# Kernel optimization log

Hardware: AMD Instinct MI355X
Metric: run time of the kernel (lower is better)

The kernel has to match this reference:

```python
import jax, jax.numpy as jnp
import numpy as np

B, L, D, H, DK, DV = 2, 2048, 1024, 16, 64, 64
NEG_INF = -100000000.0


def setup_inputs() -> dict:
    key = jax.random.key(0)
    ks = jax.random.split(key, 10)
    s = 0.02
    inp = {
        "q": jax.random.normal(ks[0], (B, L, D), jnp.float32),
        "k": jax.random.normal(ks[1], (B, L, D), jnp.float32),
        "v": jax.random.normal(ks[2], (B, L, D), jnp.float32),
        "Wq": jax.random.normal(ks[3], (D, H * DK), jnp.float32) * s,
        "bq": jnp.zeros((H * DK,), jnp.float32),
        "Wk": jax.random.normal(ks[4], (D, H * DK), jnp.float32) * s,
        "bk": jnp.zeros((H * DK,), jnp.float32),
        "Wv": jax.random.normal(ks[5], (D, H * DV), jnp.float32) * s,
        "bv": jnp.zeros((H * DV,), jnp.float32),
        "W0": jax.random.normal(ks[6], (H * DV, D), jnp.float32) * s,
        "b0": jnp.zeros((D,), jnp.float32),
        "key_padding_mask": jax.random.uniform(ks[7], (B, L)) < 0.1,
        # 3D causal mask (B, Lq, Lk); True = masked
        "attn_mask": jnp.broadcast_to(jnp.triu(jnp.ones((L, L), bool), k=1), (B, L, L)),
    }
    return inp


def reference(q, k, v, Wq, bq, Wk, bk, Wv, bv, W0, b0, key_padding_mask, attn_mask):
    b, lq, _ = q.shape
    lk = k.shape[1]
    dk = Wq.shape[1] // H
    dv = Wv.shape[1] // H
    qh = (q @ Wq + bq).reshape(b, lq, H, dk)  # (B,Lq,H,dk)
    kh = (k @ Wk + bk).reshape(b, lk, H, dk)
    vh = (v @ Wv + bv).reshape(b, lk, H, dv)
    # scaled scores (B,H,Lq,Lk)
    attn = jnp.einsum("bqhd,bkhd->bhqk", qh, kh) / jnp.sqrt(jnp.float32(dk))
    # attn_mask (B,Lq,Lk): masked_fill semantics
    attn = jnp.where(attn_mask[:, None, :, :], NEG_INF, attn)
    # key_padding_mask (B,Lq): masks full query rows (broadcast over keys)
    attn = jnp.where(key_padding_mask[:, None, :, None], NEG_INF, attn)
    attn = jax.nn.softmax(attn, axis=-1)
    out = jnp.einsum("bhqk,bkhd->bqhd", attn, vh).reshape(b, lq, H * dv)
    out = out @ W0 + b0  # (B,Lq,D)
    return out, attn
```

## Files before the change

### kernel.cpp

```cpp
#include <hip/hip_runtime.h>

#define B_ 2
#define L_ 2048
#define D_ 1024
#define H_ 16
#define DKV 64
#define NEG_INF -1e8f

typedef float f32x4 __attribute__((ext_vector_type(4)));
typedef __bf16 bf16x8 __attribute__((ext_vector_type(8)));
typedef unsigned int u32x4 __attribute__((ext_vector_type(4)));
typedef unsigned int u32x2 __attribute__((ext_vector_type(2)));
typedef unsigned short u16x4 __attribute__((ext_vector_type(4)));

__device__ __forceinline__ unsigned short f2bfbits(float f) {
  unsigned int u = __builtin_bit_cast(unsigned int, f);
  unsigned int r = (u + 0x7FFFu + ((u >> 16) & 1u)) >> 16;
  return (unsigned short)r;
}
__device__ __forceinline__ float bf2f(unsigned short b) {
  unsigned int u = ((unsigned int)b) << 16;
  return __builtin_bit_cast(float, u);
}

__device__ __forceinline__ void gload16(const unsigned short* g, unsigned short* l) {
  __builtin_amdgcn_global_load_lds(
      (const __attribute__((address_space(1))) unsigned int*)g,
      (__attribute__((address_space(3))) unsigned int*)l, 16, 0, 0);
}

template<int N>
__device__ __forceinline__ void waitbar() {
  asm volatile("s_waitcnt vmcnt(%0) lgkmcnt(0)" :: "i"(N) : "memory");
  __builtin_amdgcn_sched_barrier(0);
  __builtin_amdgcn_s_barrier();
}
__device__ __forceinline__ void bar_lgkm() {
  asm volatile("s_waitcnt lgkmcnt(0)" ::: "memory");
  __builtin_amdgcn_sched_barrier(0);
  __builtin_amdgcn_s_barrier();
}

__global__ __launch_bounds__(256) void prep_k(
    const float* __restrict__ xq, const float* __restrict__ xk, const float* __restrict__ xv,
    const float* __restrict__ Wq, const float* __restrict__ Wk,
    const float* __restrict__ Wv, const float* __restrict__ W0,
    const void* __restrict__ kpm_raw,
    unsigned short* __restrict__ oq, unsigned short* __restrict__ ok, unsigned short* __restrict__ ov,
    unsigned short* __restrict__ Wtq, unsigned short* __restrict__ Wtk,
    unsigned short* __restrict__ Wtv, unsigned short* __restrict__ W0t,
    unsigned char* __restrict__ kpmn)
{
  __shared__ float Tl[64][65];
  const int bid = blockIdx.x, tid = threadIdx.x;
  if (bid < 6144) {
    const int proj = bid >> 11;
    const float* X = proj == 0 ? xq : (proj == 1 ? xk : xv);
    unsigned short* O = proj == 0 ? oq : (proj == 1 ? ok : ov);
    const long i8 = ((long)(bid & 2047) * 256 + tid) * 8;
    f32x4 a = *(const f32x4*)(X + i8);
    f32x4 b = *(const f32x4*)(X + i8 + 4);
    u32x4 p;
    p[0] = (unsigned)f2bfbits(a[0]) | ((unsigned)f2bfbits(a[1]) << 16);
    p[1] = (unsigned)f2bfbits(a[2]) | ((unsigned)f2bfbits(a[3]) << 16);
    p[2] = (unsigned)f2bfbits(b[0]) | ((unsigned)f2bfbits(b[1]) << 16);
    p[3] = (unsigned)f2bfbits(b[2]) | ((unsigned)f2bfbits(b[3]) << 16);
    *(u32x4*)(O + i8) = p;
  } else if (bid < 7168) {
    const int wid = bid - 6144;
    const int m = wid >> 8, t = wid & 255;
    const float* W = m == 0 ? Wq : (m == 1 ? Wk : (m == 2 ? Wv : W0));
    unsigned short* Wt = m == 0 ? Wtq : (m == 1 ? Wtk : (m == 2 ? Wtv : W0t));
    const int k0 = ((t >> 4) & 15) * 64, n0 = (t & 15) * 64;
    #pragma unroll
    for (int it = 0; it < 4; ++it) {
      int idx = it * 256 + tid;
      int r = idx >> 4, c4 = (idx & 15) << 2;
      f32x4 x = *(const f32x4*)(W + (long)(k0 + r) * 1024 + n0 + c4);
      Tl[r][c4] = x[0]; Tl[r][c4 + 1] = x[1]; Tl[r][c4 + 2] = x[2]; Tl[r][c4 + 3] = x[3];
    }
    __syncthreads();
    #pragma unroll
    for (int it = 0; it < 2; ++it) {
      int idx = it * 256 + tid;
      int n = idx >> 3, c8 = (idx & 7) << 3;
      u32x4 p;
      #pragma unroll
      for (int j = 0; j < 4; ++j)
        p[j] = (unsigned)f2bfbits(Tl[c8 + 2 * j][n]) | ((unsigned)f2bfbits(Tl[c8 + 2 * j + 1][n]) << 16);
      *(u32x4*)(Wt + (long)(n0 + n) * 1024 + k0 + c8) = p;
    }
  } else {
    __shared__ int flag;
    if (tid == 0) flag = 0;
    __syncthreads();
    const unsigned* w = (const unsigned*)kpm_raw;
    unsigned bad = 0;
    for (int i = tid; i < 1024; i += 256) bad |= (w[i] > 1u) ? 1u : 0u;
    if (bad) flag = 1;
    __syncthreads();
    const bool u8 = (flag != 0);
    const unsigned char* u = (const unsigned char*)kpm_raw;
    for (int i = tid; i < B_ * L_; i += 256)
      kpmn[i] = u8 ? (u[i] != 0) : (w[i] != 0);
  }
}

__global__ __launch_bounds__(256) void qkv_gemm_k(
    const unsigned short* __restrict__ xqb, const unsigned short* __restrict__ xkb,
    const unsigned short* __restrict__ xvb,
    const unsigned short* __restrict__ Wtq, const unsigned short* __restrict__ Wtk,
    const unsigned short* __restrict__ Wtv,
    const float* __restrict__ bq, const float* __restrict__ bk, const float* __restrict__ bv,
    unsigned short* __restrict__ oq, unsigned short* __restrict__ ok, unsigned short* __restrict__ ov,
    float* __restrict__ part)
{
  __shared__ __align__(16) unsigned short Al[128][64];
  __shared__ __align__(16) unsigned short Bl[128][64];
  const int proj = blockIdx.y;
  const unsigned short* X  = proj == 0 ? xqb : (proj == 1 ? xkb : xvb);
  const unsigned short* Wt = proj == 0 ? Wtq : (proj == 1 ? Wtk : Wtv);
  const float* bias = proj == 0 ? bq : (proj == 1 ? bk : bv);
  unsigned short* O = proj == 0 ? oq : (proj == 1 ? ok : ov);
  const int mt = blockIdx.x, zp = blockIdx.z;
  const int bb = zp >> 3, hp = zp & 7;
  const int tid = threadIdx.x, lane = tid & 63, w = tid >> 6, g = lane >> 4, l16 = lane & 15;
  const int wm = w >> 1, wn = w & 1;
  const long arow0 = (long)bb * L_ + mt * 128;
  const long brow0 = (long)hp * 128;
  const int lr8 = lane >> 3, lc = lane & 7;

  const f32x4 zero4 = {0.f, 0.f, 0.f, 0.f};
  f32x4 acc[4][4];
  #pragma unroll
  for (int i = 0; i < 4; ++i)
    #pragma unroll
    for (int j = 0; j < 4; ++j) acc[i][j] = zero4;

  for (int kt = 0; kt < D_; kt += 64) {
    #pragma unroll
    for (int i = 0; i < 4; ++i) {
      int r = w * 32 + i * 8 + lr8;
      gload16(X + (arow0 + r) * D_ + kt + ((lc ^ (r & 7)) << 3), &Al[w * 32 + i * 8][0]);
      gload16(Wt + (brow0 + r) * D_ + kt + ((lc ^ (r & 7)) << 3), &Bl[w * 32 + i * 8][0]);
    }
    __syncthreads();
    #pragma unroll
    for (int ks = 0; ks < 2; ++ks) {
      bf16x8 a[4], bv8[4];
      #pragma unroll
      for (int fm = 0; fm < 4; ++fm) {
        int ra = wm * 64 + fm * 16 + l16;
        a[fm] = *(const bf16x8*)&Al[ra][((ks * 4 + g) ^ (ra & 7)) << 3];
      }
      #pragma unroll
      for (int fn = 0; fn < 4; ++fn) {
        int rb = wn * 64 + fn * 16 + l16;
        bv8[fn] = *(const bf16x8*)&Bl[rb][((ks * 4 + g) ^ (rb & 7)) << 3];
      }
      #pragma unroll
      for (int fm = 0; fm < 4; ++fm)
        #pragma unroll
        for (int fn = 0; fn < 4; ++fn)
          acc[fm][fn] = __builtin_amdgcn_mfma_f32_16x16x32_bf16(a[fm], bv8[fn], acc[fm][fn], 0, 0, 0);
    }
    __syncthreads();
  }
  #pragma unroll
  for (int fm = 0; fm < 4; ++fm)
    #pragma unroll
    for (int fn = 0; fn < 4; ++fn)
      #pragma unroll
      for (int r = 0; r < 4; ++r) {
        int row = mt * 128 + wm * 64 + fm * 16 + g * 4 + r;
        int col = wn * 64 + fn * 16 + l16;
        float val = acc[fm][fn][r] + bias[hp * 128 + col];
        int zh = bb * H_ + hp * 2 + (col >> 6);
        O[(long)zh * L_ * 64 + (long)row * 64 + (col & 63)] = f2bfbits(val);
      }

  if (proj == 2) {
    float* red = (float*)&Al[0][0];
    __syncthreads();
    #pragma unroll
    for (int fn = 0; fn < 4; ++fn) {
      float s = 0.f;
      #pragma unroll
      for (int fm = 0; fm < 4; ++fm)
        #pragma unroll
        for (int r = 0; r < 4; ++r) s += acc[fm][fn][r];
      red[(wm * 4 + g) * 128 + wn * 64 + fn * 16 + l16] = s;
    }
    __syncthreads();
    if (tid < 128) {
      float s = 0.f;
      #pragma unroll
      for (int i = 0; i < 8; ++i) s += red[i * 128 + tid];
      s += 128.f * bias[hp * 128 + tid];
      int zh = bb * H_ + hp * 2 + (tid >> 6);
      part[((long)zh * 16 + mt) * 64 + (tid & 63)] = s;
    }
  }
}

__global__ __launch_bounds__(256) void oproj_gemm_k(
    const unsigned short* __restrict__ Ab, const unsigned short* __restrict__ W0t,
    const float* __restrict__ b0, float* __restrict__ out)
{
  __shared__ __align__(16) unsigned short Al[64][64];
  __shared__ __align__(16) unsigned short Bl[64][64];
  const int mt = blockIdx.x, nt = blockIdx.y;
  const int tid = threadIdx.x, lane = tid & 63, w = tid >> 6, g = lane >> 4, l16 = lane & 15;
  const int wm = w >> 1, wn = w & 1;
  const int lr8 = lane >> 3, lc = lane & 7;

  const f32x4 zero4 = {0.f, 0.f, 0.f, 0.f};
  f32x4 acc[2][2];
  #pragma unroll
  for (int i = 0; i < 2; ++i)
    #pragma unroll
    for (int j = 0; j < 2; ++j) acc[i][j] = zero4;

  for (int kt = 0; kt < D_; kt += 64) {
    #pragma unroll
    for (int i = 0; i < 2; ++i) {
      int r = w * 16 + i * 8 + lr8;
      gload16(Ab + (long)(mt * 64 + r) * D_ + kt + ((lc ^ (r & 7)) << 3), &Al[w * 16 + i * 8][0]);
      gload16(W0t + (long)(nt * 64 + r) * D_ + kt + ((lc ^ (r & 7)) << 3), &Bl[w * 16 + i * 8][0]);
    }
    __syncthreads();
    #pragma unroll
    for (int ks = 0; ks < 2; ++ks) {
      bf16x8 a[2], bv8[2];
      #pragma unroll
      for (int fm = 0; fm < 2; ++fm) {
        int ra = wm * 32 + fm * 16 + l16;
        a[fm] = *(const bf16x8*)&Al[ra][((ks * 4 + g) ^ (ra & 7)) << 3];
      }
      #pragma unroll
      for (int fn = 0; fn < 2; ++fn) {
        int rb = wn * 32 + fn * 16 + l16;
        bv8[fn] = *(const bf16x8*)&Bl[rb][((ks * 4 + g) ^ (rb & 7)) << 3];
      }
      #pragma unroll
      for (int fm = 0; fm < 2; ++fm)
        #pragma unroll
        for (int fn = 0; fn < 2; ++fn)
          acc[fm][fn] = __builtin_amdgcn_mfma_f32_16x16x32_bf16(a[fm], bv8[fn], acc[fm][fn], 0, 0, 0);
    }
    __syncthreads();
  }
  #pragma unroll
  for (int fm = 0; fm < 2; ++fm)
    #pragma unroll
    for (int fn = 0; fn < 2; ++fn)
      #pragma unroll
      for (int r = 0; r < 4; ++r) {
        int row = mt * 64 + wm * 32 + fm * 16 + g * 4 + r;
        int col = nt * 64 + wn * 32 + fn * 16 + l16;
        out[(long)row * D_ + col] = acc[fm][fn][r] + b0[col];
      }
}

__global__ __launch_bounds__(256, 4) void attn_pv_k(
    const unsigned short* __restrict__ qh, const unsigned short* __restrict__ kh,
    const unsigned short* __restrict__ vh, const unsigned char* __restrict__ kpm,
    const float* __restrict__ part, float* __restrict__ attn,
    unsigned short* __restrict__ oh)
{
  __shared__ __align__(16) char smem[64 * 68 * 4];
  auto Ql = (unsigned short (*)[72])smem;
  auto Pl = (float (*)[68])smem;
  __shared__ __align__(16) unsigned short Kl[64][64];
  __shared__ __align__(16) unsigned short Vl[64][72];
  __shared__ unsigned char padl[64];
  __shared__ float csVl[64];

  const int tid = threadIdx.x, lane = tid & 63, w = tid >> 6, g = lane >> 4, l16 = lane & 15;
  const int bid = blockIdx.x;
  const int z = bid & 31;
  const int qq5 = bid >> 5;
  const int sx = (qq5 & 8) ? ((qq5 & 16) ? 55 - qq5 : 23 - qq5) : qq5;
  const int q0 = sx * 64;
  const int b = z >> 4, h = z & 15;
  const long zoff = (long)z * L_ * DKV;
  const int rowbase = q0 + w * 16 + g * 4;

  const int lr8 = lane >> 3, lc = lane & 7;
  const int kr = tid >> 3, kc8 = (tid & 7) << 3;
  const int vk = tid >> 4, vn4 = (tid & 15) << 2;

  #pragma unroll
  for (int it = 0; it < 2; ++it) {
    int f = it * 256 + tid;
    int r = f >> 3, c8 = (f & 7) << 3;
    *(u32x4*)&Ql[r][c8] = *(const u32x4*)(qh + zoff + (long)(q0 + r) * 64 + c8);
  }
  if (tid < 64) {
    padl[tid] = kpm[b * L_ + q0 + tid];
    float s = 0.f;
    #pragma unroll
    for (int m = 0; m < 16; ++m) s += part[((long)z * 16 + m) * 64 + tid];
    csVl[tid] = s;
  }
  __syncthreads();
  bf16x8 a[2];
  #pragma unroll
  for (int ks = 0; ks < 2; ++ks)
    a[ks] = *(const bf16x8*)&Ql[w * 16 + l16][ks * 32 + g * 8];
  bool pad[4];
  #pragma unroll
  for (int r = 0; r < 4; ++r) pad[r] = padl[w * 16 + g * 4 + r] != 0;
  __syncthreads();

  const float invL = 1.0f / (float)L_;

  float psum[4] = {0.f, 0.f, 0.f, 0.f};
  const f32x4 zero4 = {0.f, 0.f, 0.f, 0.f};
  f32x4 o[4];
  #pragma unroll
  for (int fn = 0; fn < 4; ++fn) o[fn] = zero4;

  u16x4 Vreg[4];
  #pragma unroll
  for (int it = 0; it < 4; ++it)
    Vreg[it] = *(const u16x4*)(vh + zoff + (long)(vk + it * 16) * 64 + vn4);
  #pragma unroll
  for (int it = 0; it < 4; ++it) {
    int kk = vk + it * 16;
    int sw = kk ^ (((vn4 >> 2) & 7) << 3);
    Vl[vn4 + 0][sw] = Vreg[it][0]; Vl[vn4 + 1][sw] = Vreg[it][1];
    Vl[vn4 + 2][sw] = Vreg[it][2]; Vl[vn4 + 3][sw] = Vreg[it][3];
  }
  #pragma unroll
  for (int i = 0; i < 2; ++i) {
    int r = w * 16 + i * 8 + lr8;
    gload16(kh + zoff + (long)r * 64 + ((lc ^ (r & 7)) << 3), &Kl[w * 16 + i * 8][0]);
  }
  __builtin_amdgcn_sched_barrier(0);
  if (sx >= 1)
    #pragma unroll
    for (int it = 0; it < 4; ++it)
      Vreg[it] = *(const u16x4*)(vh + zoff + (long)(64 + vk + it * 16) * 64 + vn4);

  for (int kt = 0; kt <= sx; ++kt) {
    if (kt == 0) waitbar<0>(); else waitbar<4>();
    f32x4 s[4];
    #pragma unroll
    for (int fn = 0; fn < 4; ++fn) {
      int fk = fn * 16 + l16;
      bf16x8 bv0 = *(const bf16x8*)&Kl[fk][(g ^ (fk & 7)) << 3];
      bf16x8 bv1 = *(const bf16x8*)&Kl[fk][((4 + g) ^ (fk & 7)) << 3];
      f32x4 t = zero4;
      t = __builtin_amdgcn_mfma_f32_16x16x32_bf16(a[0], bv0, t, 0, 0, 0);
      t = __builtin_amdgcn_mfma_f32_16x16x32_bf16(a[1], bv1, t, 0, 0, 0);
      s[fn] = t;
    }
    #pragma unroll
    for (int fn = 0; fn < 4; ++fn)
      #pragma unroll
      for (int r = 0; r < 4; ++r) {
        int kk = kt * 64 + fn * 16 + l16;
        float sv = s[fn][r] * 0.125f;
        if (kk > rowbase + r) sv = NEG_INF;
        float p = __expf(sv - 12.0f);
        psum[r] += p;
        Pl[w * 16 + g * 4 + r][fn * 16 + l16] = p;
      }
    bf16x8 pa[2];
    #pragma unroll
    for (int ks = 0; ks < 2; ++ks) {
      f32x4 lo = *(const f32x4*)&Pl[w * 16 + l16][ks * 32 + g * 8];
      f32x4 hi = *(const f32x4*)&Pl[w * 16 + l16][ks * 32 + g * 8 + 4];
      bf16x8 t;
      #pragma unroll
      for (int i = 0; i < 4; ++i) { t[i] = (__bf16)lo[i]; t[i + 4] = (__bf16)hi[i]; }
      pa[ks] = t;
    }
    #pragma unroll
    for (int fn = 0; fn < 4; ++fn) {
      int dv = fn * 16 + l16;
      int swz = ((dv >> 2) & 7) << 3;
      bf16x8 vb0 = *(const bf16x8*)&Vl[dv][(0 * 32 + g * 8) ^ swz];
      bf16x8 vb1 = *(const bf16x8*)&Vl[dv][(1 * 32 + g * 8) ^ swz];
      o[fn] = __builtin_amdgcn_mfma_f32_16x16x32_bf16(pa[0], vb0, o[fn], 0, 0, 0);
      o[fn] = __builtin_amdgcn_mfma_f32_16x16x32_bf16(pa[1], vb1, o[fn], 0, 0, 0);
    }
    bar_lgkm();
    if (kt < sx) {
      const unsigned short* kb2 = kh + zoff + (long)((kt + 1) * 64) * 64;
      #pragma unroll
      for (int i = 0; i < 2; ++i) {
        int r = w * 16 + i * 8 + lr8;
        gload16(kb2 + (long)r * 64 + ((lc ^ (r & 7)) << 3), &Kl[w * 16 + i * 8][0]);
      }
      __builtin_amdgcn_sched_barrier(0);
      #pragma unroll
      for (int it = 0; it < 4; ++it) {
        int kk = vk + it * 16;
        int sw = kk ^ (((vn4 >> 2) & 7) << 3);
        Vl[vn4 + 0][sw] = Vreg[it][0]; Vl[vn4 + 1][sw] = Vreg[it][1];
        Vl[vn4 + 2][sw] = Vreg[it][2]; Vl[vn4 + 3][sw] = Vreg[it][3];
      }
      if (kt + 2 <= sx) {
        const long noff = zoff + (long)((kt + 2) * 64) * 64;
        #pragma unroll
        for (int it = 0; it < 4; ++it)
          Vreg[it] = *(const u16x4*)(vh + noff + (long)(vk + it * 16) * 64 + vn4);
      }
      __builtin_amdgcn_sched_barrier(0);
    }
    {
      int dt = sx + 1 + kt;
      if (dt < L_ / 64) {
        #pragma unroll
        for (int it = 0; it < 4; ++it) {
          int f = it * 256 + tid;
          int r = f >> 4, c4 = (f & 15) << 2;
          float vvv = padl[r] ? invL : 0.f;
          f32x4 ov = {vvv, vvv, vvv, vvv};
          __builtin_nontemporal_store(ov, (f32x4*)&attn[((long)z * L_ + q0 + r) * L_ + dt * 64 + c4]);
        }
      }
    }
  }

  float linv[4], lbias[4];
  #pragma unroll
  for (int r = 0; r < 4; ++r) {
    float s = psum[r];
    #pragma unroll
    for (int d = 1; d < 16; d <<= 1) s += __shfl_xor(s, d);
    linv[r] = 1.f / s;
    lbias[r] = __logf(linv[r]) - 12.0f;
  }

  #pragma unroll
  for (int fn = 0; fn < 4; ++fn)
    #pragma unroll
    for (int r = 0; r < 4; ++r) {
      int qq = rowbase + r;
      int dv = fn * 16 + l16;
      float val = pad[r] ? invL * csVl[dv] : o[fn][r] * linv[r];
      oh[((long)b * L_ + qq) * (H_ * DKV) + h * DKV + dv] = f2bfbits(val);
    }

  u32x4 K2reg[2];
  #pragma unroll
  for (int i = 0; i < 2; ++i) {
    int r = w * 16 + i * 8 + lr8;
    gload16(kh + zoff + (long)r * 64 + ((lc ^ (r & 7)) << 3), &Kl[w * 16 + i * 8][0]);
  }
  __builtin_amdgcn_sched_barrier(0);
  if (1 <= sx) {
    #pragma unroll
    for (int it = 0; it < 2; ++it)
      K2reg[it] = *(const u32x4*)(kh + zoff + (long)(64 + kr + it * 32) * 64 + kc8);
    #pragma unroll
    for (int it = 0; it < 2; ++it)
      *(u32x4*)&Vl[kr + it * 32][kc8] = K2reg[it];
    if (3 <= sx)
      #pragma unroll
      for (int it = 0; it < 2; ++it)
        K2reg[it] = *(const u32x4*)(kh + zoff + (long)(3 * 64 + kr + it * 32) * 64 + kc8);
  }

  for (int kt = 0; kt <= sx; kt += 2) {
    const bool has2 = (kt + 1 <= sx);
    if (kt == 0) waitbar<0>(); else waitbar<8>();
    f32x4 st1[4], st2[4];
    #pragma unroll
    for (int fn = 0; fn < 4; ++fn) {
      int fk = fn * 16 + l16;
      bf16x8 bv0 = *(const bf16x8*)&Kl[fk][(g ^ (fk & 7)) << 3];
      bf16x8 bv1 = *(const bf16x8*)&Kl[fk][((4 + g) ^ (fk & 7)) << 3];
      f32x4 t = zero4;
      t = __builtin_amdgcn_mfma_f32_16x16x32_bf16(a[0], bv0, t, 0, 0, 0);
      t = __builtin_amdgcn_mfma_f32_16x16x32_bf16(a[1], bv1, t, 0, 0, 0);
      #pragma unroll
      for (int r = 0; r < 4; ++r) {
        int kk = kt * 64 + fn * 16 + l16;
        float sv = t[r] * 0.125f;
        float p = pad[r] ? invL : __expf((kk > rowbase + r) ? NEG_INF : (sv + lbias[r]));
        Pl[w * 16 + g * 4 + r][fn * 16 + l16] = p;
      }
    }
    #pragma unroll
    for (int p = 0; p < 4; ++p)
      st1[p] = *(const f32x4*)&Pl[w * 16 + p * 4 + g][l16 << 2];
    if (has2) {
      #pragma unroll
      for (int fn = 0; fn < 4; ++fn) {
        bf16x8 bv0 = *(const bf16x8*)&Vl[fn * 16 + l16][g * 8];
        bf16x8 bv1 = *(const bf16x8*)&Vl[fn * 16 + l16][32 + g * 8];
        f32x4 t = zero4;
        t = __builtin_amdgcn_mfma_f32_16x16x32_bf16(a[0], bv0, t, 0, 0, 0);
        t = __builtin_amdgcn_mfma_f32_16x16x32_bf16(a[1], bv1, t, 0, 0, 0);
        #pragma unroll
        for (int r = 0; r < 4; ++r) {
          int kk = (kt + 1) * 64 + fn * 16 + l16;
          float sv = t[r] * 0.125f;
          float p = pad[r] ? invL : __expf((kk > rowbase + r) ? NEG_INF : (sv + lbias[r]));
          Pl[w * 16 + g * 4 + r][fn * 16 + l16] = p;
        }
      }
      #pragma unroll
      for (int p = 0; p < 4; ++p)
        st2[p] = *(const f32x4*)&Pl[w * 16 + p * 4 + g][l16 << 2];
    }
    bar_lgkm();
    if (kt + 2 <= sx) {
      const unsigned short* kb2 = kh + zoff + (long)((kt + 2) * 64) * 64;
      #pragma unroll
      for (int i = 0; i < 2; ++i) {
        int r = w * 16 + i * 8 + lr8;
        gload16(kb2 + (long)r * 64 + ((lc ^ (r & 7)) << 3), &Kl[w * 16 + i * 8][0]);
      }
      __builtin_amdgcn_sched_barrier(0);
      if (kt + 3 <= sx) {
        #pragma unroll
        for (int it = 0; it < 2; ++it)
          *(u32x4*)&Vl[kr + it * 32][kc8] = K2reg[it];
        if (kt + 5 <= sx)
          #pragma unroll
          for (int it = 0; it < 2; ++it)
            K2reg[it] = *(const u32x4*)(kh + zoff + (long)((kt + 5) * 64 + kr + it * 32) * 64 + kc8);
      }
      __builtin_amdgcn_sched_barrier(0);
    }
    #pragma unroll
    for (int p = 0; p < 4; ++p)
      __builtin_nontemporal_store(st1[p],
          (f32x4*)&attn[((long)z * L_ + q0 + w * 16 + p * 4 + g) * L_ + kt * 64 + (l16 << 2)]);
    if (has2)
      #pragma unroll
      for (int p = 0; p < 4; ++p)
        __builtin_nontemporal_store(st2[p],
            (f32x4*)&attn[((long)z * L_ + q0 + w * 16 + p * 4 + g) * L_ + (kt + 1) * 64 + (l16 << 2)]);
  }

  for (int kt = 2 * (sx + 1); kt < L_ / 64; ++kt) {
    #pragma unroll
    for (int it = 0; it < 4; ++it) {
      int f = it * 256 + tid;
      int r = f >> 4, c4 = (f & 15) << 2;
      float vvv = padl[r] ? invL : 0.f;
      f32x4 ov = {vvv, vvv, vvv, vvv};
      __builtin_nontemporal_store(ov, (f32x4*)&attn[((long)z * L_ + q0 + r) * L_ + kt * 64 + c4]);
    }
  }
}

extern "C" void kernel_launch(void* const* d_in, const int* in_sizes, int n_in,
                              void* d_out, int out_size, void* d_ws, size_t ws_size,
                              hipStream_t stream) {
  (void)in_sizes; (void)n_in; (void)out_size; (void)ws_size;
  const float* q  = (const float*)d_in[0];
  const float* k  = (const float*)d_in[1];
  const float* v  = (const float*)d_in[2];
  const float* Wq = (const float*)d_in[3];
  const float* bq = (const float*)d_in[4];
  const float* Wk = (const float*)d_in[5];
  const float* bk = (const float*)d_in[6];
  const float* Wv = (const float*)d_in[7];
  const float* bv = (const float*)d_in[8];
  const float* W0 = (const float*)d_in[9];
  const float* b0 = (const float*)d_in[10];
  const void*  kpm_raw = d_in[11];

  float* out  = (float*)d_out;
  float* attn = out + (long)B_ * L_ * D_;

  const long XE = (long)B_ * L_ * D_;
  const long HEAD_ELEMS = (long)B_ * H_ * L_ * DKV;
  unsigned short* qh  = (unsigned short*)d_ws;
  unsigned short* kh  = qh + HEAD_ELEMS;
  unsigned short* vh  = kh + HEAD_ELEMS;
  unsigned short* xqb = vh + HEAD_ELEMS;
  unsigned short* xkb = xqb + XE;
  unsigned short* xvb = xkb + XE;
  unsigned short* oh  = xqb;
  unsigned short* Wtq = xvb + XE;
  unsigned short* Wtk = Wtq + (long)D_ * D_;
  unsigned short* Wtv = Wtk + (long)D_ * D_;
  unsigned short* W0t = Wtv + (long)D_ * D_;
  float* part = (float*)(W0t + (long)D_ * D_);
  unsigned char* kpmn = (unsigned char*)(part + 32 * 16 * 64);

  dim3 blk(256);

  prep_k<<<dim3(7169), blk, 0, stream>>>(
      q, k, v, Wq, Wk, Wv, W0, kpm_raw,
      xqb, xkb, xvb, Wtq, Wtk, Wtv, W0t, kpmn);

  qkv_gemm_k<<<dim3(L_ / 128, 3, B_ * (H_ / 2)), blk, 0, stream>>>(
      xqb, xkb, xvb, Wtq, Wtk, Wtv, bq, bk, bv, qh, kh, vh, part);

  attn_pv_k<<<dim3(1024), blk, 0, stream>>>(
      qh, kh, vh, kpmn, part, attn, oh);

  oproj_gemm_k<<<dim3(B_ * L_ / 64, D_ / 64), blk, 0, stream>>>(
      oh, W0t, b0, out);
}
```

Baseline: 217.0 us.

## Double attention query tile to 128 rows with 512-thread blocks

The attention kernel now gives each block 128 query rows, spread over eight waves, instead of 64 rows over four waves, and the grid is halved. Each staged K and V tile is therefore shared by twice as many rows, so per-wave loads of K and V into shared memory are halved. The causal ordering of query blocks and the odd-tile special cases are simplified, because every block now covers an even number of key tiles. In exchange, each block needs more shared memory and there are fewer, larger blocks, which may reduce occupancy and make load balancing coarser.

```diff
diff --git a/kernel.cpp b/kernel.cpp
--- a/kernel.cpp
+++ b/kernel.cpp
@@ -262,26 +262,27 @@
       }
 }
 
-__global__ __launch_bounds__(256, 4) void attn_pv_k(
+__global__ __launch_bounds__(512, 4) void attn_pv_k(
     const unsigned short* __restrict__ qh, const unsigned short* __restrict__ kh,
     const unsigned short* __restrict__ vh, const unsigned char* __restrict__ kpm,
     const float* __restrict__ part, float* __restrict__ attn,
     unsigned short* __restrict__ oh)
 {
-  __shared__ __align__(16) char smem[64 * 68 * 4];
+  __shared__ __align__(16) char smem[128 * 68 * 4];
   auto Ql = (unsigned short (*)[72])smem;
   auto Pl = (float (*)[68])smem;
   __shared__ __align__(16) unsigned short Kl[64][64];
   __shared__ __align__(16) unsigned short Vl[64][72];
-  __shared__ unsigned char padl[64];
+  __shared__ unsigned char padl[128];
   __shared__ float csVl[64];
 
   const int tid = threadIdx.x, lane = tid & 63, w = tid >> 6, g = lane >> 4, l16 = lane & 15;
   const int bid = blockIdx.x;
   const int z = bid & 31;
-  const int qq5 = bid >> 5;
-  const int sx = (qq5 & 8) ? ((qq5 & 16) ? 55 - qq5 : 23 - qq5) : qq5;
-  const int q0 = sx * 64;
+  const int qq4 = bid >> 5;
+  const int sx = (qq4 < 8) ? qq4 : 23 - qq4;
+  const int q0 = sx * 128;
+  const int ktmax = 2 * sx + 1;
   const int b = z >> 4, h = z & 15;
   const long zoff = (long)z * L_ * DKV;
   const int rowbase = q0 + w * 16 + g * 4;
@@ -292,12 +293,12 @@
 
   #pragma unroll
   for (int it = 0; it < 2; ++it) {
-    int f = it * 256 + tid;
+    int f = it * 512 + tid;
     int r = f >> 3, c8 = (f & 7) << 3;
     *(u32x4*)&Ql[r][c8] = *(const u32x4*)(qh + zoff + (long)(q0 + r) * 64 + c8);
   }
+  if (tid < 128) padl[tid] = kpm[b * L_ + q0 + tid];
   if (tid < 64) {
-    padl[tid] = kpm[b * L_ + q0 + tid];
     float s = 0.f;
     #pragma unroll
     for (int m = 0; m < 16; ++m) s += part[((long)z * 16 + m) * 64 + tid];
@@ -321,29 +322,27 @@
   #pragma unroll
   for (int fn = 0; fn < 4; ++fn) o[fn] = zero4;
 
-  u16x4 Vreg[4];
-  #pragma unroll
-  for (int it = 0; it < 4; ++it)
-    Vreg[it] = *(const u16x4*)(vh + zoff + (long)(vk + it * 16) * 64 + vn4);
-  #pragma unroll
-  for (int it = 0; it < 4; ++it) {
-    int kk = vk + it * 16;
+  u16x4 Vreg[2];
+  #pragma unroll
+  for (int it = 0; it < 2; ++it)
+    Vreg[it] = *(const u16x4*)(vh + zoff + (long)(it * 32 + vk) * 64 + vn4);
+  #pragma unroll
+  for (int it = 0; it < 2; ++it) {
+    int kk = it * 32 + vk;
     int sw = kk ^ (((vn4 >> 2) & 7) << 3);
     Vl[vn4 + 0][sw] = Vreg[it][0]; Vl[vn4 + 1][sw] = Vreg[it][1];
     Vl[vn4 + 2][sw] = Vreg[it][2]; Vl[vn4 + 3][sw] = Vreg[it][3];
   }
-  #pragma unroll
-  for (int i = 0; i < 2; ++i) {
-    int r = w * 16 + i * 8 + lr8;
-    gload16(kh + zoff + (long)r * 64 + ((lc ^ (r & 7)) << 3), &Kl[w * 16 + i * 8][0]);
+  {
+    int r = w * 8 + lr8;
+    gload16(kh + zoff + (long)r * 64 + ((lc ^ (r & 7)) << 3), &Kl[w * 8][0]);
   }
   __builtin_amdgcn_sched_barrier(0);
-  if (sx >= 1)
-    #pragma unroll
-    for (int it = 0; it < 4; ++it)
-      Vreg[it] = *(const u16x4*)(vh + zoff + (long)(64 + vk + it * 16) * 64 + vn4);
-
-  for (int kt = 0; kt <= sx; ++kt) {
+  #pragma unroll
+  for (int it = 0; it < 2; ++it)
+    Vreg[it] = *(const u16x4*)(vh + zoff + (long)(64 + it * 32 + vk) * 64 + vn4);
+
+  for (int kt = 0; kt <= ktmax; ++kt) {
     if (kt == 0) waitbar<0>(); else waitbar<4>();
     f32x4 s[4];
     #pragma unroll
@@ -387,35 +386,34 @@
       o[fn] = __builtin_amdgcn_mfma_f32_16x16x32_bf16(pa[1], vb1, o[fn], 0, 0, 0);
     }
     bar_lgkm();
-    if (kt < sx) {
+    if (kt < ktmax) {
       const unsigned short* kb2 = kh + zoff + (long)((kt + 1) * 64) * 64;
-      #pragma unroll
-      for (int i = 0; i < 2; ++i) {
-        int r = w * 16 + i * 8 + lr8;
-        gload16(kb2 + (long)r * 64 + ((lc ^ (r & 7)) << 3), &Kl[w * 16 + i * 8][0]);
+      {
+        int r = w * 8 + lr8;
+        gload16(kb2 + (long)r * 64 + ((lc ^ (r & 7)) << 3), &Kl[w * 8][0]);
       }
       __builtin_amdgcn_sched_barrier(0);
       #pragma unroll
-      for (int it = 0; it < 4; ++it) {
-        int kk = vk + it * 16;
+      for (int it = 0; it < 2; ++it) {
+        int kk = it * 32 + vk;
         int sw = kk ^ (((vn4 >> 2) & 7) << 3);
         Vl[vn4 + 0][sw] = Vreg[it][0]; Vl[vn4 + 1][sw] = Vreg[it][1];
         Vl[vn4 + 2][sw] = Vreg[it][2]; Vl[vn4 + 3][sw] = Vreg[it][3];
       }
-      if (kt + 2 <= sx) {
+      if (kt + 2 <= ktmax) {
         const long noff = zoff + (long)((kt + 2) * 64) * 64;
         #pragma unroll
-        for (int it = 0; it < 4; ++it)
-          Vreg[it] = *(const u16x4*)(vh + noff + (long)(vk + it * 16) * 64 + vn4);
+        for (int it = 0; it < 2; ++it)
+          Vreg[it] = *(const u16x4*)(vh + noff + (long)(it * 32 + vk) * 64 + vn4);
       }
       __builtin_amdgcn_sched_barrier(0);
     }
     {
-      int dt = sx + 1 + kt;
+      int dt = ktmax + 1 + kt;
       if (dt < L_ / 64) {
         #pragma unroll
         for (int it = 0; it < 4; ++it) {
-          int f = it * 256 + tid;
+          int f = it * 512 + tid;
           int r = f >> 4, c4 = (f & 15) << 2;
           float vvv = padl[r] ? invL : 0.f;
           f32x4 ov = {vvv, vvv, vvv, vvv};
@@ -445,28 +443,18 @@
       oh[((long)b * L_ + qq) * (H_ * DKV) + h * DKV + dv] = f2bfbits(val);
     }
 
-  u32x4 K2reg[2];
-  #pragma unroll
-  for (int i = 0; i < 2; ++i) {
-    int r = w * 16 + i * 8 + lr8;
-    gload16(kh + zoff + (long)r * 64 + ((lc ^ (r & 7)) << 3), &Kl[w * 16 + i * 8][0]);
+  u32x4 K2reg;
+  {
+    int r = w * 8 + lr8;
+    gload16(kh + zoff + (long)r * 64 + ((lc ^ (r & 7)) << 3), &Kl[w * 8][0]);
   }
   __builtin_amdgcn_sched_barrier(0);
-  if (1 <= sx) {
-    #pragma unroll
-    for (int it = 0; it < 2; ++it)
-      K2reg[it] = *(const u32x4*)(kh + zoff + (long)(64 + kr + it * 32) * 64 + kc8);
-    #pragma unroll
-    for (int it = 0; it < 2; ++it)
-      *(u32x4*)&Vl[kr + it * 32][kc8] = K2reg[it];
-    if (3 <= sx)
-      #pragma unroll
-      for (int it = 0; it < 2; ++it)
-        K2reg[it] = *(const u32x4*)(kh + zoff + (long)(3 * 64 + kr + it * 32) * 64 + kc8);
-  }
-
-  for (int kt = 0; kt <= sx; kt += 2) {
-    const bool has2 = (kt + 1 <= sx);
+  K2reg = *(const u32x4*)(kh + zoff + (long)(64 + kr) * 64 + kc8);
+  *(u32x4*)&Vl[kr][kc8] = K2reg;
+  if (3 <= ktmax)
+    K2reg = *(const u32x4*)(kh + zoff + (long)(3 * 64 + kr) * 64 + kc8);
+
+  for (int kt = 0; kt <= ktmax; kt += 2) {
     if (kt == 0) waitbar<0>(); else waitbar<8>();
     f32x4 st1[4], st2[4];
     #pragma unroll
@@ -488,61 +476,51 @@
     #pragma unroll
     for (int p = 0; p < 4; ++p)
       st1[p] = *(const f32x4*)&Pl[w * 16 + p * 4 + g][l16 << 2];
-    if (has2) {
-      #pragma unroll
-      for (int fn = 0; fn < 4; ++fn) {
-        bf16x8 bv0 = *(const bf16x8*)&Vl[fn * 16 + l16][g * 8];
-        bf16x8 bv1 = *(const bf16x8*)&Vl[fn * 16 + l16][32 + g * 8];
-        f32x4 t = zero4;
-        t = __builtin_amdgcn_mfma_f32_16x16x32_bf16(a[0], bv0, t, 0, 0, 0);
-        t = __builtin_amdgcn_mfma_f32_16x16x32_bf16(a[1], bv1, t, 0, 0, 0);
-        #pragma unroll
-        for (int r = 0; r < 4; ++r) {
-          int kk = (kt + 1) * 64 + fn * 16 + l16;
-          float sv = t[r] * 0.125f;
-          float p = pad[r] ? invL : __expf((kk > rowbase + r) ? NEG_INF : (sv + lbias[r]));
-          Pl[w * 16 + g * 4 + r][fn * 16 + l16] = p;
-        }
-      }
-      #pragma unroll
-      for (int p = 0; p < 4; ++p)
-        st2[p] = *(const f32x4*)&Pl[w * 16 + p * 4 + g][l16 << 2];
-    }
+    #pragma unroll
+    for (int fn = 0; fn < 4; ++fn) {
+      bf16x8 bv0 = *(const bf16x8*)&Vl[fn * 16 + l16][g * 8];
+      bf16x8 bv1 = *(const bf16x8*)&Vl[fn * 16 + l16][32 + g * 8];
+      f32x4 t = zero4;
+      t = __builtin_amdgcn_mfma_f32_16x16x32_bf16(a[0], bv0, t, 0, 0, 0);
+      t = __builtin_amdgcn_mfma_f32_16x16x32_bf16(a[1], bv1, t, 0, 0, 0);
+      #pragma unroll
+      for (int r = 0; r < 4; ++r) {
+        int kk = (kt + 1) * 64 + fn * 16 + l16;
+        float sv = t[r] * 0.125f;
+        float p = pad[r] ? invL : __expf((kk > rowbase + r) ? NEG_INF : (sv + lbias[r]));
+        Pl[w * 16 + g * 4 + r][fn * 16 + l16] = p;
+      }
+    }
+    #pragma unroll
+    for (int p = 0; p < 4; ++p)
+      st2[p] = *(const f32x4*)&Pl[w * 16 + p * 4 + g][l16 << 2];
     bar_lgkm();
-    if (kt + 2 <= sx) {
+    if (kt + 2 <= ktmax) {
       const unsigned short* kb2 = kh + zoff + (long)((kt + 2) * 64) * 64;
-      #pragma unroll
-      for (int i = 0; i < 2; ++i) {
-        int r = w * 16 + i * 8 + lr8;
-        gload16(kb2 + (long)r * 64 + ((lc ^ (r & 7)) << 3), &Kl[w * 16 + i * 8][0]);
+      {
+        int r = w * 8 + lr8;
+        gload16(kb2 + (long)r * 64 + ((lc ^ (r & 7)) << 3), &Kl[w * 8][0]);
       }
       __builtin_amdgcn_sched_barrier(0);
-      if (kt + 3 <= sx) {
-        #pragma unroll
-        for (int it = 0; it < 2; ++it)
-          *(u32x4*)&Vl[kr + it * 32][kc8] = K2reg[it];
-        if (kt + 5 <= sx)
-          #pragma unroll
-          for (int it = 0; it < 2; ++it)
-            K2reg[it] = *(const u32x4*)(kh + zoff + (long)((kt + 5) * 64 + kr + it * 32) * 64 + kc8);
-      }
+      *(u32x4*)&Vl[kr][kc8] = K2reg;
+      if (kt + 5 <= ktmax)
+        K2reg = *(const u32x4*)(kh + zoff + (long)((kt + 5) * 64 + kr) * 64 + kc8);
       __builtin_amdgcn_sched_barrier(0);
     }
     #pragma unroll
     for (int p = 0; p < 4; ++p)
       __builtin_nontemporal_store(st1[p],
           (f32x4*)&attn[((long)z * L_ + q0 + w * 16 + p * 4 + g) * L_ + kt * 64 + (l16 << 2)]);
-    if (has2)
-      #pragma unroll
-      for (int p = 0; p < 4; ++p)
-        __builtin_nontemporal_store(st2[p],
-            (f32x4*)&attn[((long)z * L_ + q0 + w * 16 + p * 4 + g) * L_ + (kt + 1) * 64 + (l16 << 2)]);
-  }
-
-  for (int kt = 2 * (sx + 1); kt < L_ / 64; ++kt) {
+    #pragma unroll
+    for (int p = 0; p < 4; ++p)
+      __builtin_nontemporal_store(st2[p],
+          (f32x4*)&attn[((long)z * L_ + q0 + w * 16 + p * 4 + g) * L_ + (kt + 1) * 64 + (l16 << 2)]);
+  }
+
+  for (int kt = 2 * (ktmax + 1); kt < L_ / 64; ++kt) {
     #pragma unroll
     for (int it = 0; it < 4; ++it) {
-      int f = it * 256 + tid;
+      int f = it * 512 + tid;
       int r = f >> 4, c4 = (f & 15) << 2;
       float vvv = padl[r] ? invL : 0.f;
       f32x4 ov = {vvv, vvv, vvv, vvv};
@@ -596,7 +574,7 @@
   qkv_gemm_k<<<dim3(L_ / 128, 3, B_ * (H_ / 2)), blk, 0, stream>>>(
       xqb, xkb, xvb, Wtq, Wtk, Wtv, bq, bk, bv, qh, kh, vh, part);
 
-  attn_pv_k<<<dim3(1024), blk, 0, stream>>>(
+  attn_pv_k<<<dim3(512), dim3(512), 0, stream>>>(
       qh, kh, vh, kpmn, part, attn, oh);
 
   oproj_gemm_k<<<dim3(B_ * L_ / 64, D_ / 64), blk, 0, stream>>>(
```

Result: no change. 218.3 us (+0.6%).
